# Optimization experiments

Measured on AMD Instinct MI355X. Metric: run time of the kernel, lower is better.

The kernel has to match this reference:

```python
import jax, jax.numpy as jnp
from jax import lax
import numpy as np

B, IN, OUT = 32768, 512, 512


def _bit_length(a):
    # a: nonnegative int32. Smear high bit down, then popcount == bit length.
    y = a
    y = y | (y >> 1)
    y = y | (y >> 2)
    y = y | (y >> 4)
    y = y | (y >> 8)
    y = y | (y >> 16)
    return lax.population_count(y)


def trunc_top_bits(v, k=4):
    # compress_top4(|a|,|b|,4): keep top-k significant bits of each magnitude.
    a = jnp.abs(v)
    shift = jnp.maximum(_bit_length(a) - k, 0)
    t = (a >> shift) << shift
    return t * jnp.sign(v)


def setup_inputs() -> dict:
    key = jax.random.key(0)
    k1, k2, k3 = jax.random.split(key, 3)
    bound = 1.0 / np.sqrt(IN)  # matches kaiming_uniform(a=sqrt(5)) + bias bound
    x = jax.random.normal(k1, (B, IN), dtype=jnp.float32)
    weight = jax.random.uniform(k2, (OUT, IN), dtype=jnp.float32, minval=-bound, maxval=bound)
    bias = jax.random.uniform(k3, (OUT,), dtype=jnp.float32, minval=-bound, maxval=bound)
    return {"x": x, "weight": weight, "bias": bias, "weight_sf": 8, "act_sf": 6}


def reference(x, weight, bias, weight_sf, act_sf):
    # Fixed-point quantization: input / 2^{-sf} then trunc-toward-zero int cast
    xi = (x * (2.0 ** act_sf)).astype(jnp.int32)       # [B, IN]
    wi = (weight * (2.0 ** weight_sf)).astype(jnp.int32)  # [OUT, IN]
    # sign/abs decomposition + top-4-bit truncated multiply-accumulate:
    # sum_y compress_top4(|xi|,|wi|) * sign(xi)*sign(wi) == dot of signed truncs
    tx = trunc_top_bits(xi).astype(jnp.float32)
    tw = trunc_top_bits(wi).astype(jnp.float32)
    acc = jnp.einsum("bi,oi->bo", tx, tw)             # [B, OUT], exact in fp32
    scale = (2.0 ** (-act_sf)) * (2.0 ** (-weight_sf))
    return acc * scale + bias[None, :]
```

## Files before the change

kernel.cpp:

```cpp
#include <hip/hip_runtime.h>
#include <hip/hip_bf16.h>
#include <stdint.h>

#define B_DIM 32768
#define IN_DIM 512
#define OUT_DIM 512

typedef __bf16 bf16;
typedef bf16 bf16x8 __attribute__((ext_vector_type(8)));
typedef float f32x4 __attribute__((ext_vector_type(4)));

__device__ __forceinline__ uint32_t quant2(float a, float b, float scale) {
    uint32_t ua = __float_as_uint(truncf(a * scale)) & 0xFFF00000u;
    uint32_t ub = __float_as_uint(truncf(b * scale)) & 0xFFF00000u;
    return (ua >> 16) | (ub & 0xFFFF0000u);
}

__global__ void quant_kernel(const float* __restrict__ in, bf16* __restrict__ out,
                             int n4, const int* __restrict__ sf) {
    int i = blockIdx.x * blockDim.x + threadIdx.x;
    if (i >= n4) return;
    float scale = (float)(1 << *sf);
    float4 v = ((const float4*)in)[i];
    uint2 p;
    p.x = quant2(v.x, v.y, scale);
    p.y = quant2(v.z, v.w, scale);
    ((uint2*)out)[i] = p;
}

__global__ __launch_bounds__(256, 4)
void gemm_fused(const float* __restrict__ X, const bf16* __restrict__ QW,
                const float* __restrict__ bias, float* __restrict__ C,
                const int* __restrict__ wsf, const int* __restrict__ asf) {
    __shared__ bf16 As[128 * 64];
    __shared__ bf16 Bs[128 * 64];

    const int t    = threadIdx.x;
    const int w    = t >> 6;
    const int lane = t & 63;

    const int b    = blockIdx.x;
    const int xcd  = b & 7;
    const int slot = b >> 3;
    const int bm   = xcd * 32 + (slot >> 2);
    const int bn   = slot & 3;
    const int row0 = bm * 128;
    const int col0 = bn * 128;
    const int wm   = (w & 1) * 64;
    const int wn   = (w >> 1) * 64;

    const int ldr = t >> 3;
    const int ldc = (t & 7) * 8;

    const float* Xbase = X  + (size_t)row0 * IN_DIM;
    const bf16*  Wbase = QW + (size_t)col0 * IN_DIM;

    const float ascale = (float)(1 << *asf);

    f32x4 acc[4][4];
    for (int mt = 0; mt < 4; ++mt)
        for (int nt = 0; nt < 4; ++nt)
            acc[mt][nt] = 0.0f;

    for (int k0 = 0; k0 < IN_DIM; k0 += 64) {
        #pragma unroll
        for (int i = 0; i < 4; ++i) {
            const bf16* gb = Wbase + (size_t)(i * 32 + ldr) * IN_DIM + k0 + ldc;
            bf16*       lb = Bs + i * 2048 + w * 512;
            __builtin_amdgcn_global_load_lds((const __attribute__((address_space(1))) void*)gb,
                                             (__attribute__((address_space(3))) void*)lb, 16, 0, 0);
        }
        #pragma unroll
        for (int i = 0; i < 4; ++i) {
            const float* g = Xbase + (size_t)(i * 32 + ldr) * IN_DIM + k0 + ldc;
            float4 v0 = ((const float4*)g)[0];
            float4 v1 = ((const float4*)g)[1];
            uint4 p;
            p.x = quant2(v0.x, v0.y, ascale);
            p.y = quant2(v0.z, v0.w, ascale);
            p.z = quant2(v1.x, v1.y, ascale);
            p.w = quant2(v1.z, v1.w, ascale);
            *(uint4*)(As + (i * 32 + ldr) * 64 + ldc) = p;
        }
        __syncthreads();

        #pragma unroll
        for (int ks = 0; ks < 2; ++ks) {
            const int kcol = ks * 32 + (lane >> 4) * 8;
            const int arow = wm + (lane & 15);
            const int brow = wn + (lane & 15);
            bf16x8 af[4], bf[4];
            #pragma unroll
            for (int mt = 0; mt < 4; ++mt)
                af[mt] = *(const bf16x8*)(As + (arow + mt * 16) * 64 + kcol);
            #pragma unroll
            for (int nt = 0; nt < 4; ++nt)
                bf[nt] = *(const bf16x8*)(Bs + (brow + nt * 16) * 64 + kcol);
            #pragma unroll
            for (int mt = 0; mt < 4; ++mt)
                #pragma unroll
                for (int nt = 0; nt < 4; ++nt)
                    acc[mt][nt] = __builtin_amdgcn_mfma_f32_16x16x32_bf16(af[mt], bf[nt], acc[mt][nt], 0, 0, 0);
        }
        __syncthreads();
    }

    const float oscale = ldexpf(1.0f, -(*wsf + *asf));
    const int cl = lane & 15;
    const int rg = (lane >> 4) * 4;
    #pragma unroll
    for (int nt = 0; nt < 4; ++nt) {
        const int col = col0 + wn + nt * 16 + cl;
        const float bv = bias[col];
        #pragma unroll
        for (int mt = 0; mt < 4; ++mt) {
            f32x4 a = acc[mt][nt];
            #pragma unroll
            for (int r = 0; r < 4; ++r) {
                const int row = row0 + wm + mt * 16 + rg + r;
                C[(size_t)row * OUT_DIM + col] = a[r] * oscale + bv;
            }
        }
    }
}

extern "C" void kernel_launch(void* const* d_in, const int* in_sizes, int n_in,
                              void* d_out, int out_size, void* d_ws, size_t ws_size,
                              hipStream_t stream) {
    const float* x    = (const float*)d_in[0];
    const float* wgt  = (const float*)d_in[1];
    const float* bias = (const float*)d_in[2];
    const int*   wsf  = (const int*)d_in[3];
    const int*   asf  = (const int*)d_in[4];

    bf16* tw = (bf16*)d_ws;

    const int nw4 = OUT_DIM * IN_DIM / 4;
    quant_kernel<<<(nw4 + 255) / 256, 256, 0, stream>>>(wgt, tw, nw4, wsf);

    const int grid = (B_DIM / 128) * (OUT_DIM / 128);
    gemm_fused<<<grid, 256, 0, stream>>>(x, tw, bias, (float*)d_out, wsf, asf);
}
```

Measured before the change: 157.7 us.

## Register-prefetch next K tile while computing, and pad LDS rows

The GEMM main loop becomes a software pipeline. Global loads for the next K tile go into registers and are issued before the MFMA compute on the current LDS tile, then quantized and written to LDS after a barrier. LDS rows are padded from 64 to 72 bf16 to cut bank conflicts on the fragment reads, and the weight tile now uses plain register loads instead of direct global-to-LDS loads. This hides global-load latency at the cost of extra registers, so launch bounds drop to 3 waves per SIMD minimum.

```diff
diff --git a/kernel.cpp b/kernel.cpp
--- a/kernel.cpp
+++ b/kernel.cpp
@@ -5,6 +5,7 @@
 #define B_DIM 32768
 #define IN_DIM 512
 #define OUT_DIM 512
+#define PAD 72
 
 typedef __bf16 bf16;
 typedef bf16 bf16x8 __attribute__((ext_vector_type(8)));
@@ -28,12 +29,12 @@
     ((uint2*)out)[i] = p;
 }
 
-__global__ __launch_bounds__(256, 4)
+__global__ __launch_bounds__(256, 3)
 void gemm_fused(const float* __restrict__ X, const bf16* __restrict__ QW,
                 const float* __restrict__ bias, float* __restrict__ C,
                 const int* __restrict__ wsf, const int* __restrict__ asf) {
-    __shared__ bf16 As[128 * 64];
-    __shared__ bf16 Bs[128 * 64];
+    __shared__ bf16 As[128 * PAD];
+    __shared__ bf16 Bs[128 * PAD];
 
     const int t    = threadIdx.x;
     const int w    = t >> 6;
@@ -52,58 +53,74 @@
     const int ldr = t >> 3;
     const int ldc = (t & 7) * 8;
 
-    const float* Xbase = X  + (size_t)row0 * IN_DIM;
-    const bf16*  Wbase = QW + (size_t)col0 * IN_DIM;
-
+    const float* Xp = X  + (size_t)(row0 + ldr) * IN_DIM + ldc;
+    const bf16*  Wp = QW + (size_t)(col0 + ldr) * IN_DIM + ldc;
     const float ascale = (float)(1 << *asf);
 
     f32x4 acc[4][4];
+    #pragma unroll
     for (int mt = 0; mt < 4; ++mt)
+        #pragma unroll
         for (int nt = 0; nt < 4; ++nt)
             acc[mt][nt] = 0.0f;
 
-    for (int k0 = 0; k0 < IN_DIM; k0 += 64) {
+    float4 a0[4], a1[4];
+    uint4  bv[4];
+
+    auto stage = [&](int k0) {
         #pragma unroll
         for (int i = 0; i < 4; ++i) {
-            const bf16* gb = Wbase + (size_t)(i * 32 + ldr) * IN_DIM + k0 + ldc;
-            bf16*       lb = Bs + i * 2048 + w * 512;
-            __builtin_amdgcn_global_load_lds((const __attribute__((address_space(1))) void*)gb,
-                                             (__attribute__((address_space(3))) void*)lb, 16, 0, 0);
+            const float* g = Xp + (size_t)i * 32 * IN_DIM + k0;
+            a0[i] = ((const float4*)g)[0];
+            a1[i] = ((const float4*)g)[1];
+            bv[i] = *(const uint4*)(Wp + (size_t)i * 32 * IN_DIM + k0);
         }
+    };
+    auto commit = [&]() {
         #pragma unroll
         for (int i = 0; i < 4; ++i) {
-            const float* g = Xbase + (size_t)(i * 32 + ldr) * IN_DIM + k0 + ldc;
-            float4 v0 = ((const float4*)g)[0];
-            float4 v1 = ((const float4*)g)[1];
             uint4 p;
-            p.x = quant2(v0.x, v0.y, ascale);
-            p.y = quant2(v0.z, v0.w, ascale);
-            p.z = quant2(v1.x, v1.y, ascale);
-            p.w = quant2(v1.z, v1.w, ascale);
-            *(uint4*)(As + (i * 32 + ldr) * 64 + ldc) = p;
+            p.x = quant2(a0[i].x, a0[i].y, ascale);
+            p.y = quant2(a0[i].z, a0[i].w, ascale);
+            p.z = quant2(a1[i].x, a1[i].y, ascale);
+            p.w = quant2(a1[i].z, a1[i].w, ascale);
+            *(uint4*)(As + (i * 32 + ldr) * PAD + ldc) = p;
+            *(uint4*)(Bs + (i * 32 + ldr) * PAD + ldc) = bv[i];
         }
-        __syncthreads();
-
+    };
+    auto compute = [&]() {
         #pragma unroll
         for (int ks = 0; ks < 2; ++ks) {
             const int kcol = ks * 32 + (lane >> 4) * 8;
             const int arow = wm + (lane & 15);
             const int brow = wn + (lane & 15);
-            bf16x8 af[4], bf[4];
+            bf16x8 af[4], bfr[4];
             #pragma unroll
             for (int mt = 0; mt < 4; ++mt)
-                af[mt] = *(const bf16x8*)(As + (arow + mt * 16) * 64 + kcol);
+                af[mt] = *(const bf16x8*)(As + (arow + mt * 16) * PAD + kcol);
             #pragma unroll
             for (int nt = 0; nt < 4; ++nt)
-                bf[nt] = *(const bf16x8*)(Bs + (brow + nt * 16) * 64 + kcol);
+                bfr[nt] = *(const bf16x8*)(Bs + (brow + nt * 16) * PAD + kcol);
             #pragma unroll
             for (int mt = 0; mt < 4; ++mt)
                 #pragma unroll
                 for (int nt = 0; nt < 4; ++nt)
-                    acc[mt][nt] = __builtin_amdgcn_mfma_f32_16x16x32_bf16(af[mt], bf[nt], acc[mt][nt], 0, 0, 0);
+                    acc[mt][nt] = __builtin_amdgcn_mfma_f32_16x16x32_bf16(af[mt], bfr[nt], acc[mt][nt], 0, 0, 0);
         }
+    };
+
+    stage(0);
+    commit();
+    __syncthreads();
+    #pragma unroll
+    for (int k0 = 64; k0 < IN_DIM; k0 += 64) {
+        stage(k0);
+        compute();
+        __syncthreads();
+        commit();
         __syncthreads();
     }
+    compute();
 
     const float oscale = ldexpf(1.0f, -(*wsf + *asf));
     const int cl = lane & 15;
@@ -111,14 +128,14 @@
     #pragma unroll
     for (int nt = 0; nt < 4; ++nt) {
         const int col = col0 + wn + nt * 16 + cl;
-        const float bv = bias[col];
+        const float bvl = bias[col];
         #pragma unroll
         for (int mt = 0; mt < 4; ++mt) {
             f32x4 a = acc[mt][nt];
             #pragma unroll
             for (int r = 0; r < 4; ++r) {
                 const int row = row0 + wm + mt * 16 + rg + r;
-                C[(size_t)row * OUT_DIM + col] = a[r] * oscale + bv;
+                C[(size_t)row * OUT_DIM + col] = a[r] * oscale + bvl;
             }
         }
     }
```

After: 192.0 us. +21.7%, slower.

## Replace LDS-staged GEMM with register-direct global loads and no barriers

Applied to the files above, without the earlier changes.

Drops shared-memory staging and the __syncthreads barriers. Each wave now loads its A and B MFMA fragments straight from global memory into registers, quantizing X on the fly, and the block tile becomes 256x64 with each wave owning 64 rows. This removes LDS traffic and synchronisation, but data reuse now depends on L1/L2, and the global loads are uncoalesced 16-byte strided row accesses. X is read 8 times across column tiles instead of 4, and the W fragments are re-read by every wave.

```diff
diff --git a/kernel.cpp b/kernel.cpp
--- a/kernel.cpp
+++ b/kernel.cpp
@@ -28,13 +28,10 @@
     ((uint2*)out)[i] = p;
 }
 
-__global__ __launch_bounds__(256, 4)
-void gemm_fused(const float* __restrict__ X, const bf16* __restrict__ QW,
-                const float* __restrict__ bias, float* __restrict__ C,
-                const int* __restrict__ wsf, const int* __restrict__ asf) {
-    __shared__ bf16 As[128 * 64];
-    __shared__ bf16 Bs[128 * 64];
-
+__global__ __launch_bounds__(256, 3)
+void gemm_rf(const float* __restrict__ X, const bf16* __restrict__ QW,
+             const float* __restrict__ bias, float* __restrict__ C,
+             const int* __restrict__ wsf, const int* __restrict__ asf) {
     const int t    = threadIdx.x;
     const int w    = t >> 6;
     const int lane = t & 63;
@@ -42,67 +39,54 @@
     const int b    = blockIdx.x;
     const int xcd  = b & 7;
     const int slot = b >> 3;
-    const int bm   = xcd * 32 + (slot >> 2);
-    const int bn   = slot & 3;
-    const int row0 = bm * 128;
-    const int col0 = bn * 128;
-    const int wm   = (w & 1) * 64;
-    const int wn   = (w >> 1) * 64;
+    const int bm   = xcd * 16 + (slot >> 3);
+    const int bn   = slot & 7;
+    const int row0 = bm * 256 + w * 64;
+    const int col0 = bn * 64;
 
-    const int ldr = t >> 3;
-    const int ldc = (t & 7) * 8;
-
-    const float* Xbase = X  + (size_t)row0 * IN_DIM;
-    const bf16*  Wbase = QW + (size_t)col0 * IN_DIM;
+    const int rl = lane & 15;
+    const int kq = (lane >> 4) * 8;
 
     const float ascale = (float)(1 << *asf);
 
+    const float* Xr[4];
+    const bf16*  Wr[4];
+    #pragma unroll
+    for (int mt = 0; mt < 4; ++mt)
+        Xr[mt] = X + (size_t)(row0 + mt * 16 + rl) * IN_DIM + kq;
+    #pragma unroll
+    for (int nt = 0; nt < 4; ++nt)
+        Wr[nt] = QW + (size_t)(col0 + nt * 16 + rl) * IN_DIM + kq;
+
     f32x4 acc[4][4];
+    #pragma unroll
     for (int mt = 0; mt < 4; ++mt)
+        #pragma unroll
         for (int nt = 0; nt < 4; ++nt)
             acc[mt][nt] = 0.0f;
 
-    for (int k0 = 0; k0 < IN_DIM; k0 += 64) {
+    #pragma unroll 2
+    for (int k = 0; k < IN_DIM; k += 32) {
+        bf16x8 af[4], bfr[4];
         #pragma unroll
-        for (int i = 0; i < 4; ++i) {
-            const bf16* gb = Wbase + (size_t)(i * 32 + ldr) * IN_DIM + k0 + ldc;
-            bf16*       lb = Bs + i * 2048 + w * 512;
-            __builtin_amdgcn_global_load_lds((const __attribute__((address_space(1))) void*)gb,
-                                             (__attribute__((address_space(3))) void*)lb, 16, 0, 0);
+        for (int nt = 0; nt < 4; ++nt)
+            bfr[nt] = *(const bf16x8*)(Wr[nt] + k);
+        #pragma unroll
+        for (int mt = 0; mt < 4; ++mt) {
+            float4 u = *(const float4*)(Xr[mt] + k);
+            float4 v = *(const float4*)(Xr[mt] + k + 4);
+            uint4 p;
+            p.x = quant2(u.x, u.y, ascale);
+            p.y = quant2(u.z, u.w, ascale);
+            p.z = quant2(v.x, v.y, ascale);
+            p.w = quant2(v.z, v.w, ascale);
+            af[mt] = *(bf16x8*)&p;
         }
         #pragma unroll
-        for (int i = 0; i < 4; ++i) {
-            const float* g = Xbase + (size_t)(i * 32 + ldr) * IN_DIM + k0 + ldc;
-            float4 v0 = ((const float4*)g)[0];
-            float4 v1 = ((const float4*)g)[1];
-            uint4 p;
-            p.x = quant2(v0.x, v0.y, ascale);
-            p.y = quant2(v0.z, v0.w, ascale);
-            p.z = quant2(v1.x, v1.y, ascale);
-            p.w = quant2(v1.z, v1.w, ascale);
-            *(uint4*)(As + (i * 32 + ldr) * 64 + ldc) = p;
-        }
-        __syncthreads();
-
-        #pragma unroll
-        for (int ks = 0; ks < 2; ++ks) {
-            const int kcol = ks * 32 + (lane >> 4) * 8;
-            const int arow = wm + (lane & 15);
-            const int brow = wn + (lane & 15);
-            bf16x8 af[4], bf[4];
-            #pragma unroll
-            for (int mt = 0; mt < 4; ++mt)
-                af[mt] = *(const bf16x8*)(As + (arow + mt * 16) * 64 + kcol);
+        for (int mt = 0; mt < 4; ++mt)
             #pragma unroll
             for (int nt = 0; nt < 4; ++nt)
-                bf[nt] = *(const bf16x8*)(Bs + (brow + nt * 16) * 64 + kcol);
-            #pragma unroll
-            for (int mt = 0; mt < 4; ++mt)
-                #pragma unroll
-                for (int nt = 0; nt < 4; ++nt)
-                    acc[mt][nt] = __builtin_amdgcn_mfma_f32_16x16x32_bf16(af[mt], bf[nt], acc[mt][nt], 0, 0, 0);
-        }
-        __syncthreads();
+                acc[mt][nt] = __builtin_amdgcn_mfma_f32_16x16x32_bf16(af[mt], bfr[nt], acc[mt][nt], 0, 0, 0);
     }
 
     const float oscale = ldexpf(1.0f, -(*wsf + *asf));
@@ -110,14 +94,14 @@
     const int rg = (lane >> 4) * 4;
     #pragma unroll
     for (int nt = 0; nt < 4; ++nt) {
-        const int col = col0 + wn + nt * 16 + cl;
+        const int col = col0 + nt * 16 + cl;
         const float bv = bias[col];
         #pragma unroll
         for (int mt = 0; mt < 4; ++mt) {
             f32x4 a = acc[mt][nt];
             #pragma unroll
             for (int r = 0; r < 4; ++r) {
-                const int row = row0 + wm + mt * 16 + rg + r;
+                const int row = row0 + mt * 16 + rg + r;
                 C[(size_t)row * OUT_DIM + col] = a[r] * oscale + bv;
             }
         }
@@ -138,6 +122,6 @@
     const int nw4 = OUT_DIM * IN_DIM / 4;
     quant_kernel<<<(nw4 + 255) / 256, 256, 0, stream>>>(wgt, tw, nw4, wsf);
 
-    const int grid = (B_DIM / 128) * (OUT_DIM / 128);
-    gemm_fused<<<grid, 256, 0, stream>>>(x, tw, bias, (float*)d_out, wsf, asf);
+    const int grid = (B_DIM / 256) * (OUT_DIM / 64);
+    gemm_rf<<<grid, 256, 0, stream>>>(x, tw, bias, (float*)d_out, wsf, asf);
 }
```

New measurement: 226.7 us. 43.7% more time.

## Stage raw fp32 activations via direct-to-LDS loads and quantize at fragment read

Applied to the files above, without the earlier changes.

X tiles are now copied as raw fp32 straight into LDS with global_load_lds, using a padded row stride (9 and 5 16-byte units per row) to avoid bank conflicts. Quantization to bf16 happens when each wave reads its MFMA fragment, not in a register round-trip before the LDS store. The K tile drops from 64 to 32. quant2 uses a byte-permute instead of separate shifts and masks. The intent is to take the activation global loads off the VGPR path. The trade-offs are twice as many barrier-separated iterations, and each wave re-quantizing the A rows that other waves also read.

```diff
diff --git a/kernel.cpp b/kernel.cpp
--- a/kernel.cpp
+++ b/kernel.cpp
@@ -5,15 +5,17 @@
 #define B_DIM 32768
 #define IN_DIM 512
 #define OUT_DIM 512
+#define BK 32
 
 typedef __bf16 bf16;
 typedef bf16 bf16x8 __attribute__((ext_vector_type(8)));
 typedef float f32x4 __attribute__((ext_vector_type(4)));
 
 __device__ __forceinline__ uint32_t quant2(float a, float b, float scale) {
-    uint32_t ua = __float_as_uint(truncf(a * scale)) & 0xFFF00000u;
-    uint32_t ub = __float_as_uint(truncf(b * scale)) & 0xFFF00000u;
-    return (ua >> 16) | (ub & 0xFFFF0000u);
+    uint32_t ua = __float_as_uint(truncf(a * scale));
+    uint32_t ub = __float_as_uint(truncf(b * scale));
+    uint32_t p = __builtin_amdgcn_perm(ub, ua, 0x07060302u);
+    return p & 0xFFF0FFF0u;
 }
 
 __global__ void quant_kernel(const float* __restrict__ in, bf16* __restrict__ out,
@@ -32,8 +34,9 @@
 void gemm_fused(const float* __restrict__ X, const bf16* __restrict__ QW,
                 const float* __restrict__ bias, float* __restrict__ C,
                 const int* __restrict__ wsf, const int* __restrict__ asf) {
-    __shared__ bf16 As[128 * 64];
-    __shared__ bf16 Bs[128 * 64];
+    __shared__ char smem[32768];
+    float* As = (float*)smem;
+    bf16*  Bs = (bf16*)(smem + 20480);
 
     const int t    = threadIdx.x;
     const int w    = t >> 6;
@@ -49,59 +52,75 @@
     const int wm   = (w & 1) * 64;
     const int wn   = (w >> 1) * 64;
 
-    const int ldr = t >> 3;
-    const int ldc = (t & 7) * 8;
-
-    const float* Xbase = X  + (size_t)row0 * IN_DIM;
-    const bf16*  Wbase = QW + (size_t)col0 * IN_DIM;
+    int srcA[5], dstA[5];
+    #pragma unroll
+    for (int i = 0; i < 5; ++i) {
+        int p  = i * 256 + t;
+        int m  = p / 9;  if (m > 127) m = 127;
+        int r  = p - m * 9;
+        int ku = (r >= 8) ? 0 : r;
+        srcA[i] = (row0 + m) * IN_DIM + ku * 4;
+        dstA[i] = p * 16;
+    }
+    int srcB[3], dstB[3];
+    #pragma unroll
+    for (int i = 0; i < 3; ++i) {
+        int p  = i * 256 + t;
+        int m  = p / 5;  if (m > 127) m = 127;
+        int r  = p - m * 5;
+        int ku = (r >= 4) ? 0 : r;
+        srcB[i] = (col0 + m) * IN_DIM + ku * 8;
+        dstB[i] = p * 16;
+    }
 
     const float ascale = (float)(1 << *asf);
+    const int q  = lane >> 4;
+    const int rl = lane & 15;
 
     f32x4 acc[4][4];
+    #pragma unroll
     for (int mt = 0; mt < 4; ++mt)
+        #pragma unroll
         for (int nt = 0; nt < 4; ++nt)
             acc[mt][nt] = 0.0f;
 
-    for (int k0 = 0; k0 < IN_DIM; k0 += 64) {
+    for (int k0 = 0; k0 < IN_DIM; k0 += BK) {
         #pragma unroll
-        for (int i = 0; i < 4; ++i) {
-            const bf16* gb = Wbase + (size_t)(i * 32 + ldr) * IN_DIM + k0 + ldc;
-            bf16*       lb = Bs + i * 2048 + w * 512;
-            __builtin_amdgcn_global_load_lds((const __attribute__((address_space(1))) void*)gb,
-                                             (__attribute__((address_space(3))) void*)lb, 16, 0, 0);
+        for (int i = 0; i < 5; ++i)
+            __builtin_amdgcn_global_load_lds(
+                (const __attribute__((address_space(1))) void*)(X + srcA[i] + k0),
+                (__attribute__((address_space(3))) void*)(smem + dstA[i]), 16, 0, 0);
+        #pragma unroll
+        for (int i = 0; i < 3; ++i)
+            __builtin_amdgcn_global_load_lds(
+                (const __attribute__((address_space(1))) void*)(QW + srcB[i] + k0),
+                (__attribute__((address_space(3))) void*)(smem + 20480 + dstB[i]), 16, 0, 0);
+        __syncthreads();
+
+        bf16x8 af[4], bfr[4];
+        #pragma unroll
+        for (int mt = 0; mt < 4; ++mt) {
+            const int m = wm + mt * 16 + rl;
+            const float* p = As + (9 * m + 2 * q) * 4;
+            f32x4 u = *(const f32x4*)p;
+            f32x4 v = *(const f32x4*)(p + 4);
+            uint4 pk;
+            pk.x = quant2(u[0], u[1], ascale);
+            pk.y = quant2(u[2], u[3], ascale);
+            pk.z = quant2(v[0], v[1], ascale);
+            pk.w = quant2(v[2], v[3], ascale);
+            af[mt] = *(bf16x8*)&pk;
         }
         #pragma unroll
-        for (int i = 0; i < 4; ++i) {
-            const float* g = Xbase + (size_t)(i * 32 + ldr) * IN_DIM + k0 + ldc;
-            float4 v0 = ((const float4*)g)[0];
-            float4 v1 = ((const float4*)g)[1];
-            uint4 p;
-            p.x = quant2(v0.x, v0.y, ascale);
-            p.y = quant2(v0.z, v0.w, ascale);
-            p.z = quant2(v1.x, v1.y, ascale);
-            p.w = quant2(v1.z, v1.w, ascale);
-            *(uint4*)(As + (i * 32 + ldr) * 64 + ldc) = p;
+        for (int nt = 0; nt < 4; ++nt) {
+            const int c = wn + nt * 16 + rl;
+            bfr[nt] = *(const bf16x8*)(Bs + (5 * c + q) * 8);
         }
-        __syncthreads();
-
         #pragma unroll
-        for (int ks = 0; ks < 2; ++ks) {
-            const int kcol = ks * 32 + (lane >> 4) * 8;
-            const int arow = wm + (lane & 15);
-            const int brow = wn + (lane & 15);
-            bf16x8 af[4], bf[4];
-            #pragma unroll
-            for (int mt = 0; mt < 4; ++mt)
-                af[mt] = *(const bf16x8*)(As + (arow + mt * 16) * 64 + kcol);
+        for (int mt = 0; mt < 4; ++mt)
             #pragma unroll
             for (int nt = 0; nt < 4; ++nt)
-                bf[nt] = *(const bf16x8*)(Bs + (brow + nt * 16) * 64 + kcol);
-            #pragma unroll
-            for (int mt = 0; mt < 4; ++mt)
-                #pragma unroll
-                for (int nt = 0; nt < 4; ++nt)
-                    acc[mt][nt] = __builtin_amdgcn_mfma_f32_16x16x32_bf16(af[mt], bf[nt], acc[mt][nt], 0, 0, 0);
-        }
+                acc[mt][nt] = __builtin_amdgcn_mfma_f32_16x16x32_bf16(af[mt], bfr[nt], acc[mt][nt], 0, 0, 0);
         __syncthreads();
     }
 
```

Result: slower. 162.4 us (+2.9%).
